# Kernel tuning notes

Measured on AMD Instinct MI355X. Metric: run time of the kernel, lower is better.

## Reference

```python
import jax, jax.numpy as jnp
import numpy as np

B, Q, H, HKV, D = 4, 1024, 32, 8, 128
HID = H * D            # 4096
BS = 16                # block_size
BLOCKS_PER_SEQ = Q // BS  # 64
NB = B * BLOCKS_PER_SEQ   # 256 total cache blocks
THETA = 10000.0
SCALE = D ** -0.5


def _rope(x, pos):
    # x: [T, h, D] (NeoX half-split rotary), pos: [T] int
    inv = 1.0 / (THETA ** (jnp.arange(0, D, 2, dtype=jnp.float32) / D))  # [D/2]
    ang = pos[:, None].astype(jnp.float32) * inv                          # [T, D/2]
    cos = jnp.cos(ang)[:, None, :]
    sin = jnp.sin(ang)[:, None, :]
    x1, x2 = jnp.split(x, 2, axis=-1)
    return jnp.concatenate([x1 * cos - x2 * sin, x1 * sin + x2 * cos], axis=-1).astype(x.dtype)


def setup_inputs() -> dict:
    key = jax.random.key(0)
    ks = jax.random.split(key, 3)
    hidden_states = jax.random.normal(ks[0], (B * Q, HID), dtype=jnp.float32)
    w_qkv = jax.random.normal(ks[1], (HID, (H + 2 * HKV) * D), dtype=jnp.float32) * 0.02
    w_o = jax.random.normal(ks[2], (H * D, HID), dtype=jnp.float32) * 0.02
    key_cache = jnp.zeros((NB, BS, HKV, D), dtype=jnp.float32)
    value_cache = jnp.zeros((NB, BS, HKV, D), dtype=jnp.float32)
    positions = jnp.tile(jnp.arange(Q, dtype=jnp.int32), B)          # context_len=0 prefill
    slot_mapping = jnp.arange(B * Q, dtype=jnp.int32)                # contiguous slots
    block_tables = jnp.arange(NB, dtype=jnp.int32).reshape(B, BLOCKS_PER_SEQ)
    return {"hidden_states": hidden_states, "w_qkv": w_qkv, "w_o": w_o,
            "key_cache": key_cache, "value_cache": value_cache,
            "positions": positions, "slot_mapping": slot_mapping,
            "block_tables": block_tables}


def reference(hidden_states, w_qkv, w_o, key_cache, value_cache, positions, slot_mapping, block_tables):
    # QKV projection and split (q_size = H*D, kv_size = HKV*D)
    qkv = hidden_states @ w_qkv
    q, k, v = jnp.split(qkv, [H * D, H * D + HKV * D], axis=-1)
    q = q.reshape(-1, H, D)
    k = k.reshape(-1, HKV, D)
    v = v.reshape(-1, HKV, D)
    q = _rope(q, positions)
    k = _rope(k, positions)
    # BlockedKVCache.write: slot -> (slot // BS, slot % BS); flatten block dims
    kc = key_cache.reshape(NB * BS, HKV, D).at[slot_mapping].set(k)
    vc = value_cache.reshape(NB * BS, HKV, D).at[slot_mapping].set(v)
    # BlockedKVCache.gather via block_table: [B, blocks, BS, HKV, D] -> [B, S, HKV, D]
    gk = kc.reshape(NB, BS, HKV, D)[block_tables].reshape(B, Q, HKV, D)
    gv = vc.reshape(NB, BS, HKV, D)[block_tables].reshape(B, Q, HKV, D)
    # repeat_kv (GQA): each kv head repeated consecutively
    rep = H // HKV
    gk = jnp.repeat(gk, rep, axis=2)   # [B, S, H, D]
    gv = jnp.repeat(gv, rep, axis=2)
    qb = q.reshape(B, Q, H, D)
    scores = jnp.einsum('bqhd,bshd->bhqs', qb, gk) * SCALE
    # visible = context_len + token_idx + 1 with context_len=0 -> causal mask
    causal = jnp.arange(Q)[None, :] <= jnp.arange(Q)[:, None]          # [q, s]
    scores = jnp.where(causal[None, None], scores.astype(jnp.float32), -jnp.inf)
    probs = jax.nn.softmax(scores, axis=-1).astype(qb.dtype)
    attn = jnp.einsum('bhqs,bshd->bqhd', probs, gv).reshape(B * Q, H * D)
    return attn @ w_o
```

## Files before the change

kernel.cpp:

```cpp
#include <hip/hip_runtime.h>
#include <stdint.h>

typedef short short8  __attribute__((ext_vector_type(8)));
typedef short short4v __attribute__((ext_vector_type(4)));
typedef float f32x4   __attribute__((ext_vector_type(4)));

#define B_    4
#define Q_    1024
#define H_    32
#define HKV_  8
#define D_    128
#define HID_  4096
#define NQKV_ 6144
#define SCALE_ 0.08838834764831845f

__device__ __forceinline__ short f2bf(float f) {
  unsigned u = __builtin_bit_cast(unsigned, f);
  u += 0x7fffu + ((u >> 16) & 1u);
  return (short)(u >> 16);
}
__device__ __forceinline__ float bf2f(short s) {
  unsigned u = ((unsigned)(unsigned short)s) << 16;
  return __builtin_bit_cast(float, u);
}

__device__ __forceinline__ void gload_lds16(const void* g, void* l) {
  __builtin_amdgcn_global_load_lds(
      (__attribute__((address_space(1))) void*)(uintptr_t)(g),
      (__attribute__((address_space(3))) void*)(l), 16, 0, 0);
}

__device__ __forceinline__ f32x4 mfma16x16x32(short8 a, short8 b, f32x4 c) {
  return __builtin_amdgcn_mfma_f32_16x16x32_bf16(a, b, c, 0, 0, 0);
}

__global__ __launch_bounds__(256) void k_cvt(const float* __restrict__ src,
                                             short* __restrict__ dst, int n) {
  int i = (blockIdx.x * 256 + threadIdx.x) * 4;
  if (i + 3 < n) {
    float4 v = *reinterpret_cast<const float4*>(src + i);
    short4v o;
    o[0] = f2bf(v.x); o[1] = f2bf(v.y); o[2] = f2bf(v.z); o[3] = f2bf(v.w);
    *reinterpret_cast<short4v*>(dst + i) = o;
  }
}

__global__ __launch_bounds__(256) void k_cvt_t(const float* __restrict__ src,
                                               short* __restrict__ dst, int R, int C) {
  __shared__ float tile[32][33];
  int c0 = blockIdx.x * 32, r0 = blockIdx.y * 32;
  int tx = threadIdx.x & 31, ty = threadIdx.x >> 5;
#pragma unroll
  for (int i = 0; i < 4; ++i)
    tile[ty + i * 8][tx] = src[(size_t)(r0 + ty + i * 8) * C + c0 + tx];
  __syncthreads();
#pragma unroll
  for (int i = 0; i < 4; ++i)
    dst[(size_t)(c0 + ty + i * 8) * R + r0 + tx] = f2bf(tile[tx][ty + i * 8]);
}

__global__ __launch_bounds__(256) void k_vt(const short* __restrict__ kv,
                                            short* __restrict__ vt) {
  __shared__ short tile[32][33];
  const int bh = blockIdx.z;
  const int s0 = blockIdx.x * 32, d0 = blockIdx.y * 32;
  const int tx = threadIdx.x & 31, ty = threadIdx.x >> 5;
  const int b = bh >> 3, hkv = bh & 7;
  const short* src = kv + (size_t)(b * Q_) * 2048 + 1024 + hkv * D_;
#pragma unroll
  for (int i = 0; i < 4; ++i)
    tile[ty + i * 8][tx] = src[(size_t)(s0 + ty + i * 8) * 2048 + d0 + tx];
  __syncthreads();
  short* dst = vt + (size_t)bh * 128 * 1024;
#pragma unroll
  for (int i = 0; i < 4; ++i)
    dst[(size_t)(d0 + ty + i * 8) * 1024 + s0 + tx] = tile[tx][ty + i * 8];
}

__global__ __launch_bounds__(256) void k_gemm1(const short* __restrict__ A,
                                               const short* __restrict__ Bt,
                                               short* __restrict__ qout,
                                               short* __restrict__ kvout) {
  __shared__ alignas(16) short Asm[2][128 * 32];
  __shared__ alignas(16) short Bsm[2][128 * 32];
  const int tid = threadIdx.x;
  const int wave = tid >> 6, lane = tid & 63;
  const int G = lane >> 4, r = lane & 15;
  const int wm = wave >> 1, wn = wave & 1;
  const size_t Arow0 = (size_t)blockIdx.y * 128;
  const size_t Brow0 = (size_t)blockIdx.x * 128;
  const int K = HID_;
  const int ldrow = lane >> 2, ldcol = (lane & 3) * 8;
  short* Cb; size_t ldc, cb;
  if (Brow0 < (size_t)HID_) { Cb = qout; ldc = HID_; cb = Brow0; }
  else                      { Cb = kvout; ldc = 2048; cb = Brow0 - HID_; }
  f32x4 acc[4][4] = {};
  for (int k0 = 0; k0 < K; k0 += 64) {
    __syncthreads();
#pragma unroll
    for (int h = 0; h < 2; ++h)
#pragma unroll
      for (int i = 0; i < 2; ++i) {
        int c = wave * 2 + i;
        gload_lds16(A + (Arow0 + c * 16 + ldrow) * K + k0 + h * 32 + ldcol, &Asm[h][c * 512]);
        gload_lds16(Bt + (Brow0 + c * 16 + ldrow) * K + k0 + h * 32 + ldcol, &Bsm[h][c * 512]);
      }
    asm volatile("s_waitcnt vmcnt(0)" ::: "memory");
    __syncthreads();
#pragma unroll
    for (int h = 0; h < 2; ++h) {
      short8 af[4], bf[4];
#pragma unroll
      for (int i = 0; i < 4; ++i)
        af[i] = *reinterpret_cast<const short8*>(&Asm[h][(wm * 64 + i * 16 + r) * 32 + G * 8]);
#pragma unroll
      for (int j = 0; j < 4; ++j)
        bf[j] = *reinterpret_cast<const short8*>(&Bsm[h][(wn * 64 + j * 16 + r) * 32 + G * 8]);
#pragma unroll
      for (int i = 0; i < 4; ++i)
#pragma unroll
        for (int j = 0; j < 4; ++j)
          acc[i][j] = mfma16x16x32(af[i], bf[j], acc[i][j]);
    }
  }
#pragma unroll
  for (int i = 0; i < 4; ++i)
#pragma unroll
    for (int j = 0; j < 4; ++j)
#pragma unroll
      for (int rr = 0; rr < 4; ++rr) {
        size_t row = Arow0 + wm * 64 + i * 16 + G * 4 + rr;
        size_t col = cb + wn * 64 + j * 16 + r;
        Cb[row * ldc + col] = f2bf(acc[i][j][rr]);
      }
}

__global__ __launch_bounds__(256) void k_gemm2(const short* __restrict__ A,
                                               const short* __restrict__ Bt,
                                               float* __restrict__ C) {
  __shared__ alignas(16) short Asm[2][128 * 32];
  __shared__ alignas(16) short Bsm[2][128 * 32];
  const int tid = threadIdx.x;
  const int wave = tid >> 6, lane = tid & 63;
  const int G = lane >> 4, r = lane & 15;
  const int wm = wave >> 1, wn = wave & 1;
  const size_t Arow0 = (size_t)blockIdx.y * 128;
  const size_t Brow0 = (size_t)blockIdx.x * 128;
  const int K = HID_;
  const int ldrow = lane >> 2, ldcol = (lane & 3) * 8;
  f32x4 acc[4][4] = {};
  for (int k0 = 0; k0 < K; k0 += 64) {
    __syncthreads();
#pragma unroll
    for (int h = 0; h < 2; ++h)
#pragma unroll
      for (int i = 0; i < 2; ++i) {
        int c = wave * 2 + i;
        gload_lds16(A + (Arow0 + c * 16 + ldrow) * K + k0 + h * 32 + ldcol, &Asm[h][c * 512]);
        gload_lds16(Bt + (Brow0 + c * 16 + ldrow) * K + k0 + h * 32 + ldcol, &Bsm[h][c * 512]);
      }
    asm volatile("s_waitcnt vmcnt(0)" ::: "memory");
    __syncthreads();
#pragma unroll
    for (int h = 0; h < 2; ++h) {
      short8 af[4], bf[4];
#pragma unroll
      for (int i = 0; i < 4; ++i)
        af[i] = *reinterpret_cast<const short8*>(&Asm[h][(wm * 64 + i * 16 + r) * 32 + G * 8]);
#pragma unroll
      for (int j = 0; j < 4; ++j)
        bf[j] = *reinterpret_cast<const short8*>(&Bsm[h][(wn * 64 + j * 16 + r) * 32 + G * 8]);
#pragma unroll
      for (int i = 0; i < 4; ++i)
#pragma unroll
        for (int j = 0; j < 4; ++j)
          acc[i][j] = mfma16x16x32(af[i], bf[j], acc[i][j]);
    }
  }
#pragma unroll
  for (int i = 0; i < 4; ++i)
#pragma unroll
    for (int j = 0; j < 4; ++j)
#pragma unroll
      for (int rr = 0; rr < 4; ++rr) {
        size_t row = Arow0 + wm * 64 + i * 16 + G * 4 + rr;
        size_t col = Brow0 + wn * 64 + j * 16 + r;
        C[row * (size_t)HID_ + col] = acc[i][j][rr];
      }
}

__global__ __launch_bounds__(256) void k_rope2(short* __restrict__ q,
                                               short* __restrict__ kv) {
  const int t = blockIdx.x;
  const float pos = (float)(t & (Q_ - 1));
  short* qrow = q + (size_t)t * HID_;
  short* krow = kv + (size_t)t * 2048;
  for (int i = threadIdx.x; i < (H_ + HKV_) * 64; i += 256) {
    int h = i >> 6, j = i & 63;
    short* row = (h < H_) ? (qrow + h * D_) : (krow + (h - H_) * D_);
    float fr = powf(10000.0f, -(float)j * (1.0f / 64.0f));
    float sn, cs;
    sincosf(pos * fr, &sn, &cs);
    float x1 = bf2f(row[j]);
    float x2 = bf2f(row[64 + j]);
    row[j]      = f2bf(x1 * cs - x2 * sn);
    row[64 + j] = f2bf(x1 * sn + x2 * cs);
  }
}

__global__ __launch_bounds__(256) void k_attn(const short* __restrict__ qbf,
                                              const short* __restrict__ kv,
                                              const short* __restrict__ vt,
                                              short* __restrict__ attn) {
  const int qt = blockIdx.x;
  const int h  = blockIdx.y;
  const int b  = blockIdx.z;
  const int hkv = h >> 2;
  const int tid = threadIdx.x, wave = tid >> 6, lane = tid & 63;
  const int G = lane >> 4, r = lane & 15;
  const int q0w = qt * 64 + wave * 16;
  const float NEG_INF = -__builtin_inff();
  __shared__ alignas(16) short Ksm[32 * 136];
  __shared__ alignas(16) short Vsm[128 * 40];
  __shared__ alignas(16) short Psm[4][16][40];
  short8 qf[4];
  {
    const short* qrow = qbf + ((size_t)(b * Q_ + q0w + r)) * HID_ + h * D_;
#pragma unroll
    for (int ds = 0; ds < 4; ++ds)
      qf[ds] = *reinterpret_cast<const short8*>(qrow + ds * 32 + G * 8);
  }
  f32x4 acc[8] = {};
  float m_run = NEG_INF, l_run = 0.f;
  const int ntiles = qt * 2 + 2;
  const int my_q = q0w + r;
  const int my_q_hi = q0w + 15;
  const int krow = tid >> 3, kd0 = (tid & 7) * 16;
  const int vd = tid >> 2, vsc = (tid & 3) * 8;
  const short* vt_base = vt + (size_t)(b * 8 + hkv) * 128 * 1024;
  uint4 kreg0, kreg1, vreg0, vreg1;
  auto preload = [&](int st) {
    const short* gk = kv + ((size_t)(b * Q_ + st * 32 + krow)) * 2048 + hkv * D_ + kd0;
    kreg0 = *reinterpret_cast<const uint4*>(gk);
    kreg1 = *reinterpret_cast<const uint4*>(gk + 8);
    vreg0 = *reinterpret_cast<const uint4*>(vt_base + (size_t)vd * 1024 + st * 32 + vsc);
    vreg1 = *reinterpret_cast<const uint4*>(vt_base + (size_t)(vd + 64) * 1024 + st * 32 + vsc);
  };
  preload(0);
  for (int st = 0; st < ntiles; ++st) {
    __syncthreads();
    {
      *reinterpret_cast<uint4*>(&Ksm[krow * 136 + kd0])     = kreg0;
      *reinterpret_cast<uint4*>(&Ksm[krow * 136 + kd0 + 8]) = kreg1;
      *reinterpret_cast<uint4*>(&Vsm[vd * 40 + vsc])        = vreg0;
      *reinterpret_cast<uint4*>(&Vsm[(vd + 64) * 40 + vsc]) = vreg1;
    }
    __syncthreads();
    if (st + 1 < ntiles) preload(st + 1);
    if (st * 32 <= my_q_hi) {
      f32x4 sacc[2] = {};
      __builtin_amdgcn_s_setprio(1);
#pragma unroll
      for (int sb = 0; sb < 2; ++sb)
#pragma unroll
        for (int ds = 0; ds < 4; ++ds) {
          short8 kf = *reinterpret_cast<const short8*>(&Ksm[(sb * 16 + r) * 136 + ds * 32 + G * 8]);
          sacc[sb] = mfma16x16x32(kf, qf[ds], sacc[sb]);
        }
      __builtin_amdgcn_s_setprio(0);
      float vals[8];
      float mymax = NEG_INF;
#pragma unroll
      for (int sb = 0; sb < 2; ++sb)
#pragma unroll
        for (int j = 0; j < 4; ++j) {
          int sIdx = st * 32 + sb * 16 + G * 4 + j;
          float v = sacc[sb][j] * SCALE_;
          v = (sIdx <= my_q) ? v : NEG_INF;
          vals[sb * 4 + j] = v;
          mymax = fmaxf(mymax, v);
        }
      mymax = fmaxf(mymax, __shfl_xor(mymax, 16));
      mymax = fmaxf(mymax, __shfl_xor(mymax, 32));
      float m_new = fmaxf(m_run, mymax);
      float factor = __expf(m_run - m_new);
      float psum = 0.f;
      float pv_[8];
#pragma unroll
      for (int i = 0; i < 8; ++i) {
        float p = __expf(vals[i] - m_new);
        psum += p;
        pv_[i] = p;
      }
      psum += __shfl_xor(psum, 16);
      psum += __shfl_xor(psum, 32);
      l_run = l_run * factor + psum;
      m_run = m_new;
#pragma unroll
      for (int i = 0; i < 8; ++i)
        Psm[wave][r][(i >> 2) * 16 + G * 4 + (i & 3)] = f2bf(pv_[i]);
      asm volatile("s_waitcnt lgkmcnt(0)" ::: "memory");
      __builtin_amdgcn_sched_barrier(0);
      short8 pf = *reinterpret_cast<const short8*>(&Psm[wave][r][G * 8]);
      float frow[4];
#pragma unroll
      for (int rr = 0; rr < 4; ++rr) frow[rr] = __shfl(factor, G * 4 + rr);
#pragma unroll
      for (int dt = 0; dt < 8; ++dt)
#pragma unroll
        for (int rr = 0; rr < 4; ++rr) acc[dt][rr] *= frow[rr];
      __builtin_amdgcn_s_setprio(1);
#pragma unroll
      for (int dt = 0; dt < 8; ++dt) {
        short8 vf = *reinterpret_cast<const short8*>(&Vsm[(dt * 16 + r) * 40 + G * 8]);
        acc[dt] = mfma16x16x32(pf, vf, acc[dt]);
      }
      __builtin_amdgcn_s_setprio(0);
    }
  }
  float inv = 1.0f / l_run;
  float irow[4];
#pragma unroll
  for (int rr = 0; rr < 4; ++rr) irow[rr] = __shfl(inv, G * 4 + rr);
#pragma unroll
  for (int dt = 0; dt < 8; ++dt)
#pragma unroll
    for (int rr = 0; rr < 4; ++rr) {
      size_t rowi = (size_t)(b * Q_ + q0w + G * 4 + rr) * HID_;
      attn[rowi + h * D_ + dt * 16 + r] = f2bf(acc[dt][rr] * irow[rr]);
    }
}

extern "C" void kernel_launch(void* const* d_in, const int* in_sizes, int n_in,
                              void* d_out, int out_size, void* d_ws, size_t ws_size,
                              hipStream_t stream) {
  const float* hidden = (const float*)d_in[0];
  const float* w_qkv  = (const float*)d_in[1];
  const float* w_o    = (const float*)d_in[2];
  float* out = (float*)d_out;
  char* ws = (char*)d_ws;
  char* od = (char*)d_out;
  short* hid_bf  = (short*)(od + 0);
  short* q_bf    = (short*)(od + 33554432);
  short* wqkvT   = (short*)(ws + 0);
  short* kv_ws   = (short*)(ws + 50331648);
  short* v_t     = (short*)(ws + 33554432);
  short* attn_bf = (short*)(ws + 0);
  short* woT     = (short*)(ws + 33554432);

  k_cvt<<<dim3(16384), dim3(256), 0, stream>>>(hidden, hid_bf, HID_ * B_ * Q_);
  k_cvt_t<<<dim3(192, 128), dim3(256), 0, stream>>>(w_qkv, wqkvT, HID_, NQKV_);
  k_gemm1<<<dim3(48, 32), dim3(256), 0, stream>>>(hid_bf, wqkvT, q_bf, kv_ws);
  k_rope2<<<dim3(B_ * Q_), dim3(256), 0, stream>>>(q_bf, kv_ws);
  k_vt<<<dim3(32, 4, 32), dim3(256), 0, stream>>>(kv_ws, v_t);
  k_attn<<<dim3(16, 32, 4), dim3(256), 0, stream>>>(q_bf, kv_ws, v_t, attn_bf);
  k_cvt_t<<<dim3(128, 128), dim3(256), 0, stream>>>(w_o, woT, HID_, HID_);
  k_gemm2<<<dim3(32, 32), dim3(256), 0, stream>>>(attn_bf, woT, out);
}
```

Before: 650.6 us.

## Process two query heads per attention block to reuse shared K/V tiles

Each attention workgroup now handles two query heads that share the same KV head. Each K/V tile loaded into shared memory serves twice as many MFMA operations, and the grid shrinks by half along the head dimension. The cost is doubled accumulator and Q-fragment registers, which may lower occupancy, plus fewer workgroups to spread across CUs.

Result: no change. 655.4 us (+0.7%).

```diff
diff --git a/kernel.cpp b/kernel.cpp
--- a/kernel.cpp
+++ b/kernel.cpp
@@ -213,9 +213,10 @@
                                               const short* __restrict__ vt,
                                               short* __restrict__ attn) {
   const int qt = blockIdx.x;
-  const int h  = blockIdx.y;
+  const int hp = blockIdx.y;
   const int b  = blockIdx.z;
-  const int hkv = h >> 2;
+  const int h0 = hp * 2;
+  const int hkv = hp >> 1;
   const int tid = threadIdx.x, wave = tid >> 6, lane = tid & 63;
   const int G = lane >> 4, r = lane & 15;
   const int q0w = qt * 64 + wave * 16;
@@ -223,15 +224,16 @@
   __shared__ alignas(16) short Ksm[32 * 136];
   __shared__ alignas(16) short Vsm[128 * 40];
   __shared__ alignas(16) short Psm[4][16][40];
-  short8 qf[4];
-  {
-    const short* qrow = qbf + ((size_t)(b * Q_ + q0w + r)) * HID_ + h * D_;
+  short8 qf[2][4];
+#pragma unroll
+  for (int hh = 0; hh < 2; ++hh) {
+    const short* qrow = qbf + ((size_t)(b * Q_ + q0w + r)) * HID_ + (h0 + hh) * D_;
 #pragma unroll
     for (int ds = 0; ds < 4; ++ds)
-      qf[ds] = *reinterpret_cast<const short8*>(qrow + ds * 32 + G * 8);
-  }
-  f32x4 acc[8] = {};
-  float m_run = NEG_INF, l_run = 0.f;
+      qf[hh][ds] = *reinterpret_cast<const short8*>(qrow + ds * 32 + G * 8);
+  }
+  f32x4 acc[2][8] = {};
+  float m_run[2] = {NEG_INF, NEG_INF}, l_run[2] = {0.f, 0.f};
   const int ntiles = qt * 2 + 2;
   const int my_q = q0w + r;
   const int my_q_hi = q0w + 15;
@@ -258,77 +260,83 @@
     __syncthreads();
     if (st + 1 < ntiles) preload(st + 1);
     if (st * 32 <= my_q_hi) {
-      f32x4 sacc[2] = {};
-      __builtin_amdgcn_s_setprio(1);
-#pragma unroll
-      for (int sb = 0; sb < 2; ++sb)
-#pragma unroll
-        for (int ds = 0; ds < 4; ++ds) {
-          short8 kf = *reinterpret_cast<const short8*>(&Ksm[(sb * 16 + r) * 136 + ds * 32 + G * 8]);
-          sacc[sb] = mfma16x16x32(kf, qf[ds], sacc[sb]);
+#pragma unroll
+      for (int hh = 0; hh < 2; ++hh) {
+        f32x4 sacc[2] = {};
+        __builtin_amdgcn_s_setprio(1);
+#pragma unroll
+        for (int sb = 0; sb < 2; ++sb)
+#pragma unroll
+          for (int ds = 0; ds < 4; ++ds) {
+            short8 kf = *reinterpret_cast<const short8*>(&Ksm[(sb * 16 + r) * 136 + ds * 32 + G * 8]);
+            sacc[sb] = mfma16x16x32(kf, qf[hh][ds], sacc[sb]);
+          }
+        __builtin_amdgcn_s_setprio(0);
+        float vals[8];
+        float mymax = NEG_INF;
+#pragma unroll
+        for (int sb = 0; sb < 2; ++sb)
+#pragma unroll
+          for (int j = 0; j < 4; ++j) {
+            int sIdx = st * 32 + sb * 16 + G * 4 + j;
+            float v = sacc[sb][j] * SCALE_;
+            v = (sIdx <= my_q) ? v : NEG_INF;
+            vals[sb * 4 + j] = v;
+            mymax = fmaxf(mymax, v);
+          }
+        mymax = fmaxf(mymax, __shfl_xor(mymax, 16));
+        mymax = fmaxf(mymax, __shfl_xor(mymax, 32));
+        float m_new = fmaxf(m_run[hh], mymax);
+        float factor = __expf(m_run[hh] - m_new);
+        float psum = 0.f;
+        float pv_[8];
+#pragma unroll
+        for (int i = 0; i < 8; ++i) {
+          float p = __expf(vals[i] - m_new);
+          psum += p;
+          pv_[i] = p;
         }
-      __builtin_amdgcn_s_setprio(0);
-      float vals[8];
-      float mymax = NEG_INF;
-#pragma unroll
-      for (int sb = 0; sb < 2; ++sb)
-#pragma unroll
-        for (int j = 0; j < 4; ++j) {
-          int sIdx = st * 32 + sb * 16 + G * 4 + j;
-          float v = sacc[sb][j] * SCALE_;
-          v = (sIdx <= my_q) ? v : NEG_INF;
-          vals[sb * 4 + j] = v;
-          mymax = fmaxf(mymax, v);
+        psum += __shfl_xor(psum, 16);
+        psum += __shfl_xor(psum, 32);
+        l_run[hh] = l_run[hh] * factor + psum;
+        m_run[hh] = m_new;
+#pragma unroll
+        for (int i = 0; i < 8; ++i)
+          Psm[wave][r][(i >> 2) * 16 + G * 4 + (i & 3)] = f2bf(pv_[i]);
+        asm volatile("s_waitcnt lgkmcnt(0)" ::: "memory");
+        __builtin_amdgcn_sched_barrier(0);
+        short8 pf = *reinterpret_cast<const short8*>(&Psm[wave][r][G * 8]);
+        float frow[4];
+#pragma unroll
+        for (int rr = 0; rr < 4; ++rr) frow[rr] = __shfl(factor, G * 4 + rr);
+#pragma unroll
+        for (int dt = 0; dt < 8; ++dt)
+#pragma unroll
+          for (int rr = 0; rr < 4; ++rr) acc[hh][dt][rr] *= frow[rr];
+        __builtin_amdgcn_s_setprio(1);
+#pragma unroll
+        for (int dt = 0; dt < 8; ++dt) {
+          short8 vf = *reinterpret_cast<const short8*>(&Vsm[(dt * 16 + r) * 40 + G * 8]);
+          acc[hh][dt] = mfma16x16x32(pf, vf, acc[hh][dt]);
         }
-      mymax = fmaxf(mymax, __shfl_xor(mymax, 16));
-      mymax = fmaxf(mymax, __shfl_xor(mymax, 32));
-      float m_new = fmaxf(m_run, mymax);
-      float factor = __expf(m_run - m_new);
-      float psum = 0.f;
-      float pv_[8];
-#pragma unroll
-      for (int i = 0; i < 8; ++i) {
-        float p = __expf(vals[i] - m_new);
-        psum += p;
-        pv_[i] = p;
-      }
-      psum += __shfl_xor(psum, 16);
-      psum += __shfl_xor(psum, 32);
-      l_run = l_run * factor + psum;
-      m_run = m_new;
-#pragma unroll
-      for (int i = 0; i < 8; ++i)
-        Psm[wave][r][(i >> 2) * 16 + G * 4 + (i & 3)] = f2bf(pv_[i]);
-      asm volatile("s_waitcnt lgkmcnt(0)" ::: "memory");
-      __builtin_amdgcn_sched_barrier(0);
-      short8 pf = *reinterpret_cast<const short8*>(&Psm[wave][r][G * 8]);
-      float frow[4];
-#pragma unroll
-      for (int rr = 0; rr < 4; ++rr) frow[rr] = __shfl(factor, G * 4 + rr);
-#pragma unroll
-      for (int dt = 0; dt < 8; ++dt)
-#pragma unroll
-        for (int rr = 0; rr < 4; ++rr) acc[dt][rr] *= frow[rr];
-      __builtin_amdgcn_s_setprio(1);
-#pragma unroll
-      for (int dt = 0; dt < 8; ++dt) {
-        short8 vf = *reinterpret_cast<const short8*>(&Vsm[(dt * 16 + r) * 40 + G * 8]);
-        acc[dt] = mfma16x16x32(pf, vf, acc[dt]);
-      }
-      __builtin_amdgcn_s_setprio(0);
+        __builtin_amdgcn_s_setprio(0);
+      }
     }
   }
-  float inv = 1.0f / l_run;
-  float irow[4];
-#pragma unroll
-  for (int rr = 0; rr < 4; ++rr) irow[rr] = __shfl(inv, G * 4 + rr);
-#pragma unroll
-  for (int dt = 0; dt < 8; ++dt)
-#pragma unroll
-    for (int rr = 0; rr < 4; ++rr) {
-      size_t rowi = (size_t)(b * Q_ + q0w + G * 4 + rr) * HID_;
-      attn[rowi + h * D_ + dt * 16 + r] = f2bf(acc[dt][rr] * irow[rr]);
-    }
+#pragma unroll
+  for (int hh = 0; hh < 2; ++hh) {
+    float inv = 1.0f / l_run[hh];
+    float irow[4];
+#pragma unroll
+    for (int rr = 0; rr < 4; ++rr) irow[rr] = __shfl(inv, G * 4 + rr);
+#pragma unroll
+    for (int dt = 0; dt < 8; ++dt)
+#pragma unroll
+      for (int rr = 0; rr < 4; ++rr) {
+        size_t rowi = (size_t)(b * Q_ + q0w + G * 4 + rr) * HID_;
+        attn[rowi + (h0 + hh) * D_ + dt * 16 + r] = f2bf(acc[hh][dt][rr] * irow[rr]);
+      }
+  }
 }
 
 extern "C" void kernel_launch(void* const* d_in, const int* in_sizes, int n_in,
@@ -353,7 +361,7 @@
   k_gemm1<<<dim3(48, 32), dim3(256), 0, stream>>>(hid_bf, wqkvT, q_bf, kv_ws);
   k_rope2<<<dim3(B_ * Q_), dim3(256), 0, stream>>>(q_bf, kv_ws);
   k_vt<<<dim3(32, 4, 32), dim3(256), 0, stream>>>(kv_ws, v_t);
-  k_attn<<<dim3(16, 32, 4), dim3(256), 0, stream>>>(q_bf, kv_ws, v_t, attn_bf);
+  k_attn<<<dim3(16, 16, 4), dim3(256), 0, stream>>>(q_bf, kv_ws, v_t, attn_bf);
   k_cvt_t<<<dim3(128, 128), dim3(256), 0, stream>>>(w_o, woT, HID_, HID_);
   k_gemm2<<<dim3(32, 32), dim3(256), 0, stream>>>(attn_bf, woT, out);
 }
```
